# Performance work log

Measured on AMD Instinct MI355X. Metric: run time of the kernel, lower is better.

Reference implementation:

```python
import jax, jax.numpy as jnp
import numpy as np

D_MODEL = 1024
NUM_HEADS = 16
D_K = D_MODEL // NUM_HEADS


def setup_inputs() -> dict:
    key = jax.random.key(0)
    ks = jax.random.split(key, 9)
    s = 1.0 / np.sqrt(D_MODEL)
    x = jax.random.normal(ks[0], (2, 2048, D_MODEL), dtype=jnp.float32)
    Wq = jax.random.uniform(ks[1], (D_MODEL, D_MODEL), jnp.float32, -s, s)
    bq = jax.random.uniform(ks[2], (D_MODEL,), jnp.float32, -s, s)
    Wk = jax.random.uniform(ks[3], (D_MODEL, D_MODEL), jnp.float32, -s, s)
    bk = jax.random.uniform(ks[4], (D_MODEL,), jnp.float32, -s, s)
    Wv = jax.random.uniform(ks[5], (D_MODEL, D_MODEL), jnp.float32, -s, s)
    bv = jax.random.uniform(ks[6], (D_MODEL,), jnp.float32, -s, s)
    Wo = jax.random.uniform(ks[7], (D_MODEL, D_MODEL), jnp.float32, -s, s)
    bo = jax.random.uniform(ks[8], (D_MODEL,), jnp.float32, -s, s)
    return {"x": x, "Wq": Wq, "bq": bq, "Wk": Wk, "bk": bk,
            "Wv": Wv, "bv": bv, "Wo": Wo, "bo": bo}


def reference(x, Wq, bq, Wk, bk, Wv, bv, Wo, bo):
    B, S, _ = x.shape
    # projections (torch Linear: x @ W.T + b; here W stored as [in, out])
    q = (x @ Wq + bq).reshape(B, S, NUM_HEADS, D_K).transpose(0, 2, 1, 3)
    k = (x @ Wk + bk).reshape(B, S, NUM_HEADS, D_K).transpose(0, 2, 1, 3)
    v = (x @ Wv + bv).reshape(B, S, NUM_HEADS, D_K).transpose(0, 2, 1, 3)
    scores = jnp.einsum('bhqd,bhkd->bhqk', q, k) / jnp.sqrt(jnp.float32(D_K))
    attn = jax.nn.softmax(scores, axis=-1)
    out = jnp.einsum('bhqk,bhkd->bhqd', attn, v)  # [B,H,S,Dk]
    out = out.transpose(0, 2, 1, 3).reshape(B, S, D_MODEL)
    return out @ Wo + bo
```

## Files before the change

kernel.cpp:

```cpp
#include <hip/hip_runtime.h>
#include <hip/hip_bf16.h>

#define SEQ   2048
#define DM    1024
#define NH    16
#define DK    64
#define BATCH 2
#define M_TOT 4096
#define C1 0.18033688011112042f

typedef __attribute__((ext_vector_type(8))) short bf16x8;
typedef __attribute__((ext_vector_type(4))) float f32x4;
typedef unsigned short u16;

__device__ inline u16 f2b(float f) {
    union { float f; unsigned u; } x; x.f = f;
    return (u16)((x.u + 0x7FFFu + ((x.u >> 16) & 1u)) >> 16);
}

__device__ inline unsigned pk2(float a, float b) {
    __hip_bfloat162 h = __float22bfloat162_rn(make_float2(a, b));
    return *reinterpret_cast<unsigned*>(&h);
}

__device__ inline void async_cp16(const u16* g, u16* l) {
    __builtin_amdgcn_global_load_lds(
        (const __attribute__((address_space(1))) unsigned int*)g,
        (__attribute__((address_space(3))) unsigned int*)l, 16, 0, 0);
}

__global__ __launch_bounds__(256) void cast_x(
    const float4* __restrict__ x, uint2* __restrict__ xb)
{
    int gid = blockIdx.x * 256 + threadIdx.x;
    float4 v = x[gid];
    uint2 o;
    o.x = pk2(v.x, v.y); o.y = pk2(v.z, v.w);
    xb[gid] = o;
}

__global__ __launch_bounds__(256) void transpose_cast4(
    const float* __restrict__ W0, const float* __restrict__ W1,
    const float* __restrict__ W2, const float* __restrict__ W3,
    u16* __restrict__ WtBase)
{
    __shared__ float tile[32][33];
    const int t = threadIdx.x;
    const int n0 = blockIdx.x << 5, k0 = blockIdx.y << 5, z = blockIdx.z;
    const float* W = (z == 0) ? W0 : (z == 1) ? W1 : (z == 2) ? W2 : W3;
    u16* Wt = WtBase + (size_t)z * DM * DM;
    #pragma unroll
    for (int i = 0; i < 4; ++i) {
        int idx = t + (i << 8); int r = idx >> 5, c = idx & 31;
        tile[r][c] = W[(size_t)(k0 + r) * DM + n0 + c];
    }
    __syncthreads();
    #pragma unroll
    for (int i = 0; i < 4; ++i) {
        int idx = t + (i << 8); int r = idx >> 5, c = idx & 31;
        Wt[(size_t)(n0 + r) * DM + k0 + c] = f2b(tile[c][r]);
    }
}

__global__ __launch_bounds__(256) void gemm_bt(
    const u16* __restrict__ A, const u16* __restrict__ Bt, int mode,
    const float* __restrict__ bias0, const float* __restrict__ bias1,
    const float* __restrict__ bias2,
    void* __restrict__ out0, void* __restrict__ out1, void* __restrict__ out2)
{
    __shared__ u16 sh[9216];
    u16* As = sh;
    u16* Bs = sh + 4096;
    const int t = threadIdx.x, wid = t >> 6, lane = t & 63;
    const int lr = lane & 15, quad = lane >> 4;
    const int m0 = blockIdx.y << 7, n0 = blockIdx.x << 7;
    const int wm = (wid & 1) << 6, wn = (wid >> 1) << 6;
    const int rowA = lane >> 2;
    const int colA = (((lane & 3) - ((lane >> 3) & 3)) & 3) << 3;
    const int sA = (((lr >> 1) + quad) & 3) << 3;

    f32x4 acc[4][4];
    #pragma unroll
    for (int i = 0; i < 4; ++i)
        #pragma unroll
        for (int j = 0; j < 4; ++j) acc[i][j] = (f32x4){0.f, 0.f, 0.f, 0.f};

    for (int k0 = 0; k0 < DM; k0 += 32) {
        #pragma unroll
        for (int i = 0; i < 2; ++i) {
            int ch = wid * 2 + i;
            async_cp16(A  + (size_t)(m0 + ch * 16 + rowA) * DM + k0 + colA,
                       As + ch * 16 * 32);
            async_cp16(Bt + (size_t)(n0 + ch * 16 + rowA) * DM + k0 + colA,
                       Bs + ch * 16 * 32);
        }
        __syncthreads();
        bf16x8 af[4], bfr[4];
        #pragma unroll
        for (int mt = 0; mt < 4; ++mt)
            af[mt] = *(const bf16x8*)(As + (wm + 16 * mt + lr) * 32 + sA);
        #pragma unroll
        for (int nt = 0; nt < 4; ++nt)
            bfr[nt] = *(const bf16x8*)(Bs + (wn + 16 * nt + lr) * 32 + sA);
        #pragma unroll
        for (int mt = 0; mt < 4; ++mt)
            #pragma unroll
            for (int nt = 0; nt < 4; ++nt)
                acc[mt][nt] = __builtin_amdgcn_mfma_f32_16x16x32_bf16(
                    af[mt], bfr[nt], acc[mt][nt], 0, 0, 0);
        __syncthreads();
    }

    if (mode == 1) {
        u16* wstrip = sh + wid * 1152;
        const int ngb = n0 + wn;
        const int which = ngb >> 10, nnb = ngb & 1023;
        const int h = nnb >> 6;
        const float* bp = (which == 0) ? bias0 : (which == 1) ? bias1 : bias2;
        const float sc = (which == 0) ? C1 : 1.0f;
        float bias_v[4];
        #pragma unroll
        for (int nt = 0; nt < 4; ++nt) bias_v[nt] = bp[nnb + 16 * nt + lr];

        if (which != 1) {
            u16* dst = (which == 0) ? (u16*)out0 : (u16*)out2;
            #pragma unroll
            for (int mt = 0; mt < 4; ++mt) {
                #pragma unroll
                for (int nt = 0; nt < 4; ++nt) {
                    uint2 w;
                    w.x = pk2((acc[mt][nt][0] + bias_v[nt]) * sc,
                              (acc[mt][nt][1] + bias_v[nt]) * sc);
                    w.y = pk2((acc[mt][nt][2] + bias_v[nt]) * sc,
                              (acc[mt][nt][3] + bias_v[nt]) * sc);
                    *(uint2*)(wstrip + (16 * nt + lr) * 16 + quad * 4) = w;
                }
                asm volatile("s_waitcnt lgkmcnt(0)" ::: "memory");
                #pragma unroll
                for (int half = 0; half < 2; ++half) {
                    int id = lane + 64 * half;
                    int d = id >> 1, cho = (id & 1) << 3;
                    int m = m0 + wm + 16 * mt + cho;
                    int b = m >> 11, s = m & (SEQ - 1);
                    *(uint4*)(dst + ((size_t)(b * NH + h) * DK + d) * SEQ + s) =
                        *(const uint4*)(wstrip + d * 16 + cho);
                }
                asm volatile("s_waitcnt lgkmcnt(0)" ::: "memory");
            }
        } else {
            u16* dst = (u16*)out1;
            #pragma unroll
            for (int mt = 0; mt < 4; ++mt) {
                #pragma unroll
                for (int nt = 0; nt < 4; ++nt)
                    #pragma unroll
                    for (int r = 0; r < 4; ++r)
                        wstrip[(quad * 4 + r) * 72 + 16 * nt + lr] =
                            f2b(acc[mt][nt][r] + bias_v[nt]);
                asm volatile("s_waitcnt lgkmcnt(0)" ::: "memory");
                #pragma unroll
                for (int half = 0; half < 2; ++half) {
                    int id = lane + 64 * half;
                    int mloc = id >> 3, dl = (id & 7) << 3;
                    int m = m0 + wm + 16 * mt + mloc;
                    int b = m >> 11, s = m & (SEQ - 1);
                    *(uint4*)(dst + ((size_t)(b * NH + h) * SEQ + s) * DK + dl) =
                        *(const uint4*)(wstrip + mloc * 72 + dl);
                }
                asm volatile("s_waitcnt lgkmcnt(0)" ::: "memory");
            }
        }
    } else {
        float* O = (float*)out0;
        float* strip = (float*)sh + wid * 1088;
        float bias_v[4];
        #pragma unroll
        for (int nt = 0; nt < 4; ++nt) bias_v[nt] = bias0[n0 + wn + 16 * nt + lr];
        #pragma unroll
        for (int mt = 0; mt < 4; ++mt) {
            #pragma unroll
            for (int nt = 0; nt < 4; ++nt)
                #pragma unroll
                for (int r = 0; r < 4; ++r)
                    strip[(quad * 4 + r) * 68 + 16 * nt + lr] =
                        acc[mt][nt][r] + bias_v[nt];
            asm volatile("s_waitcnt lgkmcnt(0)" ::: "memory");
            #pragma unroll
            for (int rr = 0; rr < 4; ++rr) {
                int row = lane >> 2, chunk = (lane & 3) + 4 * rr;
                float4 v = *(const float4*)(strip + row * 68 + chunk * 4);
                *(float4*)(O + (size_t)(m0 + wm + 16 * mt + row) * DM
                             + n0 + wn + chunk * 4) = v;
            }
            asm volatile("s_waitcnt lgkmcnt(0)" ::: "memory");
        }
    }
}

__global__ __launch_bounds__(256) void attn_mfma(
    const u16* __restrict__ Qt, const u16* __restrict__ K,
    const u16* __restrict__ Vt, u16* __restrict__ A)
{
    __shared__ u16 sh[24576];

    const int t = threadIdx.x, wid = t >> 6, lane = t & 63;
    const int lr = lane & 15, quad = lane >> 4;
    const int bx = blockIdx.x;
    const int xcd = bx & 7, within = bx >> 3;
    const int bh  = xcd * 4 + (within >> 4);
    const int q0  = (within & 15) << 7;

    const u16* Kb = K  + (size_t)bh * SEQ * DK;
    const u16* Vb = Vt + (size_t)bh * DK * SEQ;

    const int qbase = q0 + 32 * wid + lr;
    const u16* Qb = Qt + (size_t)bh * DK * SEQ;
    bf16x8 bQ[2][2];
    #pragma unroll
    for (int g = 0; g < 2; ++g) {
        const u16* Qp = Qb + qbase + 16 * g;
        #pragma unroll
        for (int j = 0; j < 8; ++j) {
            bQ[g][0][j] = (short)Qp[(size_t)(quad * 8 + j) * SEQ];
            bQ[g][1][j] = (short)Qp[(size_t)(32 + quad * 8 + j) * SEQ];
        }
    }

    f32x4 O[2][4];
    #pragma unroll
    for (int g = 0; g < 2; ++g)
        #pragma unroll
        for (int mt = 0; mt < 4; ++mt) O[g][mt] = (f32x4){0.f, 0.f, 0.f, 0.f};
    float l_r[2] = {0.f, 0.f};

    const int srow = t >> 3;
    const int scol = (((t & 7) ^ (srow & 7)) << 3);

    const int c0 = ((quad ^ (lr & 7)) << 3);
    const int c1 = (((quad + 4) ^ (lr & 7)) << 3);
    const int prow = 16384 + wid * 2048 + lr * 64;

    auto stage = [&](int kt, int buf) {
        u16* kd = sh + (buf << 12);
        u16* vd = sh + 8192 + (buf << 12);
        async_cp16(Kb + (size_t)(kt + srow) * DK + scol,       kd + wid * 512);
        async_cp16(Kb + (size_t)(kt + srow + 32) * DK + scol,  kd + 2048 + wid * 512);
        async_cp16(Vb + (size_t)srow * SEQ + kt + scol,        vd + wid * 512);
        async_cp16(Vb + (size_t)(srow + 32) * SEQ + kt + scol, vd + 2048 + wid * 512);
    };

    stage(0, 0);
    __syncthreads();

    for (int it = 0; it < SEQ / 64; ++it) {
        const int kbase = (it & 1) << 12;
        const int vbase = 8192 + ((it & 1) << 12);
        if (it + 1 < SEQ / 64) stage((it + 1) << 6, (it + 1) & 1);

        #pragma unroll
        for (int mt = 0; mt < 4; ++mt) {
            bf16x8 a0 = *(const bf16x8*)(sh + kbase + (16 * mt + lr) * 64 + c0);
            bf16x8 a1 = *(const bf16x8*)(sh + kbase + (16 * mt + lr) * 64 + c1);
            #pragma unroll
            for (int g = 0; g < 2; ++g) {
                f32x4 s = (f32x4){0.f, 0.f, 0.f, 0.f};
                s = __builtin_amdgcn_mfma_f32_16x16x32_bf16(a0, bQ[g][0], s, 0, 0, 0);
                s = __builtin_amdgcn_mfma_f32_16x16x32_bf16(a1, bQ[g][1], s, 0, 0, 0);
                float e0 = __builtin_amdgcn_exp2f(s[0]);
                float e1 = __builtin_amdgcn_exp2f(s[1]);
                float e2 = __builtin_amdgcn_exp2f(s[2]);
                float e3 = __builtin_amdgcn_exp2f(s[3]);
                l_r[g] += (e0 + e1) + (e2 + e3);
                uint2 pk;
                pk.x = pk2(e0, e1); pk.y = pk2(e2, e3);
                int chunk = 2 * mt + (quad >> 1);
                *(uint2*)(sh + prow + (g << 10) + ((chunk ^ (lr & 7)) << 3)
                             + ((quad & 1) << 2)) = pk;
            }
        }
        asm volatile("s_waitcnt lgkmcnt(0)" ::: "memory");

        bf16x8 p00 = *(const bf16x8*)(sh + prow + c0);
        bf16x8 p01 = *(const bf16x8*)(sh + prow + c1);
        bf16x8 p10 = *(const bf16x8*)(sh + prow + 1024 + c0);
        bf16x8 p11 = *(const bf16x8*)(sh + prow + 1024 + c1);
        #pragma unroll
        for (int mt = 0; mt < 4; ++mt) {
            bf16x8 v0 = *(const bf16x8*)(sh + vbase + (16 * mt + lr) * 64 + c0);
            bf16x8 v1 = *(const bf16x8*)(sh + vbase + (16 * mt + lr) * 64 + c1);
            O[0][mt] = __builtin_amdgcn_mfma_f32_16x16x32_bf16(v0, p00, O[0][mt], 0, 0, 0);
            O[0][mt] = __builtin_amdgcn_mfma_f32_16x16x32_bf16(v1, p01, O[0][mt], 0, 0, 0);
            O[1][mt] = __builtin_amdgcn_mfma_f32_16x16x32_bf16(v0, p10, O[1][mt], 0, 0, 0);
            O[1][mt] = __builtin_amdgcn_mfma_f32_16x16x32_bf16(v1, p11, O[1][mt], 0, 0, 0);
        }
        if (it + 1 < SEQ / 64) __syncthreads();
    }

    #pragma unroll
    for (int g = 0; g < 2; ++g) {
        l_r[g] += __shfl_xor(l_r[g], 16);
        l_r[g] += __shfl_xor(l_r[g], 32);
    }

    const int b = bh >> 4, h = bh & 15;
    #pragma unroll
    for (int g = 0; g < 2; ++g) {
        float inv = 1.f / l_r[g];
        const int q = qbase + 16 * g;
        #pragma unroll
        for (int mt = 0; mt < 4; ++mt) {
            uint2 pk;
            pk.x = pk2(O[g][mt][0] * inv, O[g][mt][1] * inv);
            pk.y = pk2(O[g][mt][2] * inv, O[g][mt][3] * inv);
            *(uint2*)(A + (size_t)(b * SEQ + q) * DM + h * DK + 16 * mt + 4 * quad) = pk;
        }
    }
}

extern "C" void kernel_launch(void* const* d_in, const int* in_sizes, int n_in,
                              void* d_out, int out_size, void* d_ws, size_t ws_size,
                              hipStream_t stream)
{
    const float* x  = (const float*)d_in[0];
    const float* Wq = (const float*)d_in[1];
    const float* bq = (const float*)d_in[2];
    const float* Wk = (const float*)d_in[3];
    const float* bk = (const float*)d_in[4];
    const float* Wv = (const float*)d_in[5];
    const float* bv = (const float*)d_in[6];
    const float* Wo = (const float*)d_in[7];
    const float* bo = (const float*)d_in[8];

    const size_t NE = (size_t)M_TOT * DM;
    u16* xb     = (u16*)d_ws;
    u16* wt_qkv = xb + NE;
    u16* wt_o   = wt_qkv + 3 * (size_t)DM * DM;
    u16* qt_ws  = wt_o + (size_t)DM * DM;
    u16* k_ws   = qt_ws + NE;
    u16* vt_ws  = k_ws + NE;
    u16* a_ws   = vt_ws + NE;

    cast_x<<<M_TOT * DM / 4 / 256, 256, 0, stream>>>((const float4*)x, (uint2*)xb);
    transpose_cast4<<<dim3(32, 32, 4), 256, 0, stream>>>(Wq, Wk, Wv, Wo, wt_qkv);

    gemm_bt<<<dim3(24, 32), 256, 0, stream>>>(
        xb, wt_qkv, 1, bq, bk, bv, qt_ws, k_ws, vt_ws);

    attn_mfma<<<dim3(512), 256, 0, stream>>>(qt_ws, k_ws, vt_ws, a_ws);

    gemm_bt<<<dim3(8, 32), 256, 0, stream>>>(
        a_ws, wt_o, 0, bo, nullptr, nullptr, d_out, nullptr, nullptr);
}
```

Baseline: 217.3 us.

## Software-pipeline attention loop: overlap previous tile's PV MFMA with current QK

Restructures the attention main loop so each iteration first runs the P·V MFMAs for the previous tile, then the Q·K MFMAs for the current tile, with exp and the P write deferred until afterwards. The P buffer is double-buffered and V is triple-buffered to hold the extra tile in flight, with a final epilogue for the last PV step. s_setprio is raised around the MFMA block. The aim is to hide the exp/LDS-write latency behind matrix work and drop the mid-iteration lgkmcnt wait. In exchange it uses more LDS (72KB) and more registers, which may reduce occupancy.

Result: no change. 213.3 us (-1.8%).

```diff
diff --git a/kernel.cpp b/kernel.cpp
--- a/kernel.cpp
+++ b/kernel.cpp
@@ -201,7 +201,7 @@
     const u16* __restrict__ Qt, const u16* __restrict__ K,
     const u16* __restrict__ Vt, u16* __restrict__ A)
 {
-    __shared__ u16 sh[24576];
+    __shared__ u16 sh[36864];
 
     const int t = threadIdx.x, wid = t >> 6, lane = t & 63;
     const int lr = lane & 15, quad = lane >> 4;
@@ -238,62 +238,110 @@
 
     const int c0 = ((quad ^ (lr & 7)) << 3);
     const int c1 = (((quad + 4) ^ (lr & 7)) << 3);
-    const int prow = 16384 + wid * 2048 + lr * 64;
-
-    auto stage = [&](int kt, int buf) {
-        u16* kd = sh + (buf << 12);
-        u16* vd = sh + 8192 + (buf << 12);
+    const int pwave = 20480 + wid * 4096 + lr * 64;
+
+    auto stage = [&](int kt, int kbuf, int vbuf) {
+        u16* kd = sh + (kbuf << 12);
+        u16* vd = sh + 8192 + (vbuf << 12);
         async_cp16(Kb + (size_t)(kt + srow) * DK + scol,       kd + wid * 512);
         async_cp16(Kb + (size_t)(kt + srow + 32) * DK + scol,  kd + 2048 + wid * 512);
         async_cp16(Vb + (size_t)srow * SEQ + kt + scol,        vd + wid * 512);
         async_cp16(Vb + (size_t)(srow + 32) * SEQ + kt + scol, vd + 2048 + wid * 512);
     };
 
-    stage(0, 0);
+    stage(0, 0, 0);
     __syncthreads();
 
+    int vst = 1, vpv = 2;
     for (int it = 0; it < SEQ / 64; ++it) {
-        const int kbase = (it & 1) << 12;
-        const int vbase = 8192 + ((it & 1) << 12);
-        if (it + 1 < SEQ / 64) stage((it + 1) << 6, (it + 1) & 1);
-
-        #pragma unroll
-        for (int mt = 0; mt < 4; ++mt) {
-            bf16x8 a0 = *(const bf16x8*)(sh + kbase + (16 * mt + lr) * 64 + c0);
-            bf16x8 a1 = *(const bf16x8*)(sh + kbase + (16 * mt + lr) * 64 + c1);
+        if (it + 1 < SEQ / 64) stage((it + 1) << 6, (~it) & 1, vst);
+
+        bf16x8 p00, p01, p10, p11;
+        bf16x8 vf0[4], vf1[4];
+        if (it > 0) {
+            const int pr = pwave + (((~it) & 1) << 11);
+            p00 = *(const bf16x8*)(sh + pr + c0);
+            p01 = *(const bf16x8*)(sh + pr + c1);
+            p10 = *(const bf16x8*)(sh + pr + 1024 + c0);
+            p11 = *(const bf16x8*)(sh + pr + 1024 + c1);
+            const u16* vbp = sh + 8192 + (vpv << 12);
+            #pragma unroll
+            for (int mt = 0; mt < 4; ++mt) {
+                vf0[mt] = *(const bf16x8*)(vbp + (16 * mt + lr) * 64 + c0);
+                vf1[mt] = *(const bf16x8*)(vbp + (16 * mt + lr) * 64 + c1);
+            }
+        }
+
+        const u16* kbp = sh + ((it & 1) << 12);
+        bf16x8 a0[4], a1[4];
+        #pragma unroll
+        for (int mt = 0; mt < 4; ++mt) {
+            a0[mt] = *(const bf16x8*)(kbp + (16 * mt + lr) * 64 + c0);
+            a1[mt] = *(const bf16x8*)(kbp + (16 * mt + lr) * 64 + c1);
+        }
+
+        __builtin_amdgcn_s_setprio(1);
+        if (it > 0) {
+            #pragma unroll
+            for (int mt = 0; mt < 4; ++mt) {
+                O[0][mt] = __builtin_amdgcn_mfma_f32_16x16x32_bf16(vf0[mt], p00, O[0][mt], 0, 0, 0);
+                O[0][mt] = __builtin_amdgcn_mfma_f32_16x16x32_bf16(vf1[mt], p01, O[0][mt], 0, 0, 0);
+                O[1][mt] = __builtin_amdgcn_mfma_f32_16x16x32_bf16(vf0[mt], p10, O[1][mt], 0, 0, 0);
+                O[1][mt] = __builtin_amdgcn_mfma_f32_16x16x32_bf16(vf1[mt], p11, O[1][mt], 0, 0, 0);
+            }
+        }
+        f32x4 S[2][4];
+        #pragma unroll
+        for (int mt = 0; mt < 4; ++mt) {
             #pragma unroll
             for (int g = 0; g < 2; ++g) {
                 f32x4 s = (f32x4){0.f, 0.f, 0.f, 0.f};
-                s = __builtin_amdgcn_mfma_f32_16x16x32_bf16(a0, bQ[g][0], s, 0, 0, 0);
-                s = __builtin_amdgcn_mfma_f32_16x16x32_bf16(a1, bQ[g][1], s, 0, 0, 0);
-                float e0 = __builtin_amdgcn_exp2f(s[0]);
-                float e1 = __builtin_amdgcn_exp2f(s[1]);
-                float e2 = __builtin_amdgcn_exp2f(s[2]);
-                float e3 = __builtin_amdgcn_exp2f(s[3]);
+                s = __builtin_amdgcn_mfma_f32_16x16x32_bf16(a0[mt], bQ[g][0], s, 0, 0, 0);
+                s = __builtin_amdgcn_mfma_f32_16x16x32_bf16(a1[mt], bQ[g][1], s, 0, 0, 0);
+                S[g][mt] = s;
+            }
+        }
+        __builtin_amdgcn_s_setprio(0);
+
+        const int pw = pwave + ((it & 1) << 11);
+        #pragma unroll
+        for (int mt = 0; mt < 4; ++mt) {
+            #pragma unroll
+            for (int g = 0; g < 2; ++g) {
+                float e0 = __builtin_amdgcn_exp2f(S[g][mt][0]);
+                float e1 = __builtin_amdgcn_exp2f(S[g][mt][1]);
+                float e2 = __builtin_amdgcn_exp2f(S[g][mt][2]);
+                float e3 = __builtin_amdgcn_exp2f(S[g][mt][3]);
                 l_r[g] += (e0 + e1) + (e2 + e3);
                 uint2 pk;
                 pk.x = pk2(e0, e1); pk.y = pk2(e2, e3);
                 int chunk = 2 * mt + (quad >> 1);
-                *(uint2*)(sh + prow + (g << 10) + ((chunk ^ (lr & 7)) << 3)
+                *(uint2*)(sh + pw + (g << 10) + ((chunk ^ (lr & 7)) << 3)
                              + ((quad & 1) << 2)) = pk;
             }
         }
-        asm volatile("s_waitcnt lgkmcnt(0)" ::: "memory");
-
-        bf16x8 p00 = *(const bf16x8*)(sh + prow + c0);
-        bf16x8 p01 = *(const bf16x8*)(sh + prow + c1);
-        bf16x8 p10 = *(const bf16x8*)(sh + prow + 1024 + c0);
-        bf16x8 p11 = *(const bf16x8*)(sh + prow + 1024 + c1);
-        #pragma unroll
-        for (int mt = 0; mt < 4; ++mt) {
-            bf16x8 v0 = *(const bf16x8*)(sh + vbase + (16 * mt + lr) * 64 + c0);
-            bf16x8 v1 = *(const bf16x8*)(sh + vbase + (16 * mt + lr) * 64 + c1);
+
+        __syncthreads();
+        if (++vst == 3) vst = 0;
+        if (++vpv == 3) vpv = 0;
+    }
+
+    {
+        const int pr = pwave + (((SEQ / 64 - 1) & 1) << 11);
+        bf16x8 p00 = *(const bf16x8*)(sh + pr + c0);
+        bf16x8 p01 = *(const bf16x8*)(sh + pr + c1);
+        bf16x8 p10 = *(const bf16x8*)(sh + pr + 1024 + c0);
+        bf16x8 p11 = *(const bf16x8*)(sh + pr + 1024 + c1);
+        const u16* vbp = sh + 8192 + (((SEQ / 64 - 1) % 3) << 12);
+        #pragma unroll
+        for (int mt = 0; mt < 4; ++mt) {
+            bf16x8 v0 = *(const bf16x8*)(vbp + (16 * mt + lr) * 64 + c0);
+            bf16x8 v1 = *(const bf16x8*)(vbp + (16 * mt + lr) * 64 + c1);
             O[0][mt] = __builtin_amdgcn_mfma_f32_16x16x32_bf16(v0, p00, O[0][mt], 0, 0, 0);
             O[0][mt] = __builtin_amdgcn_mfma_f32_16x16x32_bf16(v1, p01, O[0][mt], 0, 0, 0);
             O[1][mt] = __builtin_amdgcn_mfma_f32_16x16x32_bf16(v0, p10, O[1][mt], 0, 0, 0);
             O[1][mt] = __builtin_amdgcn_mfma_f32_16x16x32_bf16(v1, p11, O[1][mt], 0, 0, 0);
         }
-        if (it + 1 < SEQ / 64) __syncthreads();
     }
 
     #pragma unroll
```

## Switch attention to 32x32x16 MFMA with register-resident P via permlane32 swap

Applied to the files above, without the earlier changes.

Rewrites the attention inner loop to use 32x32x16 bf16 MFMA tiles instead of 16x16x32. The softmax probabilities now stay in registers and are rearranged with permlane32_swap, so the P round-trip through LDS and its wait are gone and the LDS footprint shrinks. It also adds s_setprio around the MFMA phases. In exchange, each lane now holds larger accumulators, so register pressure rises, and the epilogue writes scalar 16-bit values through an LDS-staged row-sum table instead of packed stores.

After: 211.0 us. -2.9%, faster.

```diff
diff --git a/kernel.cpp b/kernel.cpp
--- a/kernel.cpp
+++ b/kernel.cpp
@@ -11,6 +11,8 @@
 
 typedef __attribute__((ext_vector_type(8))) short bf16x8;
 typedef __attribute__((ext_vector_type(4))) float f32x4;
+typedef __attribute__((ext_vector_type(16))) float f32x16;
+typedef __attribute__((ext_vector_type(2))) int i32x2;
 typedef unsigned short u16;
 
 __device__ inline u16 f2b(float f) {
@@ -28,6 +30,21 @@
         (const __attribute__((address_space(1))) unsigned int*)g,
         (__attribute__((address_space(3))) unsigned int*)l, 16, 0, 0);
 }
+
+__device__ inline f32x16 zero16() {
+    f32x16 z;
+    #pragma unroll
+    for (int i = 0; i < 16; ++i) z[i] = 0.f;
+    return z;
+}
+
+__device__ inline bf16x8 mk8(unsigned a, unsigned b, unsigned c, unsigned d) {
+    union { unsigned u[4]; bf16x8 v; } x;
+    x.u[0] = a; x.u[1] = b; x.u[2] = c; x.u[3] = d;
+    return x.v;
+}
+
+#define MFMA32(a, b, c) __builtin_amdgcn_mfma_f32_32x32x16_bf16(a, b, c, 0, 0, 0)
 
 __global__ __launch_bounds__(256) void cast_x(
     const float4* __restrict__ x, uint2* __restrict__ xb)
@@ -201,10 +218,10 @@
     const u16* __restrict__ Qt, const u16* __restrict__ K,
     const u16* __restrict__ Vt, u16* __restrict__ A)
 {
-    __shared__ u16 sh[24576];
+    __shared__ u16 sh[16640];
 
     const int t = threadIdx.x, wid = t >> 6, lane = t & 63;
-    const int lr = lane & 15, quad = lane >> 4;
+    const int l31 = lane & 31, hi = lane >> 5, l7 = lane & 7;
     const int bx = blockIdx.x;
     const int xcd = bx & 7, within = bx >> 3;
     const int bh  = xcd * 4 + (within >> 4);
@@ -213,32 +230,25 @@
     const u16* Kb = K  + (size_t)bh * SEQ * DK;
     const u16* Vb = Vt + (size_t)bh * DK * SEQ;
 
-    const int qbase = q0 + 32 * wid + lr;
-    const u16* Qb = Qt + (size_t)bh * DK * SEQ;
-    bf16x8 bQ[2][2];
-    #pragma unroll
-    for (int g = 0; g < 2; ++g) {
-        const u16* Qp = Qb + qbase + 16 * g;
-        #pragma unroll
-        for (int j = 0; j < 8; ++j) {
-            bQ[g][0][j] = (short)Qp[(size_t)(quad * 8 + j) * SEQ];
-            bQ[g][1][j] = (short)Qp[(size_t)(32 + quad * 8 + j) * SEQ];
-        }
-    }
-
-    f32x4 O[2][4];
-    #pragma unroll
-    for (int g = 0; g < 2; ++g)
-        #pragma unroll
-        for (int mt = 0; mt < 4; ++mt) O[g][mt] = (f32x4){0.f, 0.f, 0.f, 0.f};
-    float l_r[2] = {0.f, 0.f};
+    const int qw = q0 + 32 * wid + l31;
+    const u16* Qb = Qt + (size_t)bh * DK * SEQ + qw;
+    bf16x8 bQ[4];
+    #pragma unroll
+    for (int s = 0; s < 4; ++s)
+        #pragma unroll
+        for (int j = 0; j < 8; ++j)
+            bQ[s][j] = (short)Qb[(size_t)(16 * s + 8 * hi + j) * SEQ];
+
+    f32x16 O0 = zero16(), O1 = zero16();
+    float lr = 0.f;
 
     const int srow = t >> 3;
     const int scol = (((t & 7) ^ (srow & 7)) << 3);
 
-    const int c0 = ((quad ^ (lr & 7)) << 3);
-    const int c1 = (((quad + 4) ^ (lr & 7)) << 3);
-    const int prow = 16384 + wid * 2048 + lr * 64;
+    const int rA = l31 * 64;
+    int cks[4];
+    #pragma unroll
+    for (int s = 0; s < 4; ++s) cks[s] = ((2 * s + hi) ^ l7) << 3;
 
     auto stage = [&](int kt, int buf) {
         u16* kd = sh + (buf << 12);
@@ -253,67 +263,83 @@
     __syncthreads();
 
     for (int it = 0; it < SEQ / 64; ++it) {
-        const int kbase = (it & 1) << 12;
-        const int vbase = 8192 + ((it & 1) << 12);
+        const u16* kbp = sh + ((it & 1) << 12) + rA;
+        const u16* vbp = sh + 8192 + ((it & 1) << 12) + rA;
         if (it + 1 < SEQ / 64) stage((it + 1) << 6, (it + 1) & 1);
 
-        #pragma unroll
-        for (int mt = 0; mt < 4; ++mt) {
-            bf16x8 a0 = *(const bf16x8*)(sh + kbase + (16 * mt + lr) * 64 + c0);
-            bf16x8 a1 = *(const bf16x8*)(sh + kbase + (16 * mt + lr) * 64 + c1);
-            #pragma unroll
-            for (int g = 0; g < 2; ++g) {
-                f32x4 s = (f32x4){0.f, 0.f, 0.f, 0.f};
-                s = __builtin_amdgcn_mfma_f32_16x16x32_bf16(a0, bQ[g][0], s, 0, 0, 0);
-                s = __builtin_amdgcn_mfma_f32_16x16x32_bf16(a1, bQ[g][1], s, 0, 0, 0);
-                float e0 = __builtin_amdgcn_exp2f(s[0]);
-                float e1 = __builtin_amdgcn_exp2f(s[1]);
-                float e2 = __builtin_amdgcn_exp2f(s[2]);
-                float e3 = __builtin_amdgcn_exp2f(s[3]);
-                l_r[g] += (e0 + e1) + (e2 + e3);
-                uint2 pk;
-                pk.x = pk2(e0, e1); pk.y = pk2(e2, e3);
-                int chunk = 2 * mt + (quad >> 1);
-                *(uint2*)(sh + prow + (g << 10) + ((chunk ^ (lr & 7)) << 3)
-                             + ((quad & 1) << 2)) = pk;
+        f32x16 Sv[2];
+        __builtin_amdgcn_s_setprio(1);
+        {
+            bf16x8 a;
+            f32x16 s0 = zero16();
+            a = *(const bf16x8*)(kbp + cks[0]); s0 = MFMA32(a, bQ[0], s0);
+            a = *(const bf16x8*)(kbp + cks[1]); s0 = MFMA32(a, bQ[1], s0);
+            a = *(const bf16x8*)(kbp + cks[2]); s0 = MFMA32(a, bQ[2], s0);
+            a = *(const bf16x8*)(kbp + cks[3]); s0 = MFMA32(a, bQ[3], s0);
+            Sv[0] = s0;
+            f32x16 s1 = zero16();
+            a = *(const bf16x8*)(kbp + 2048 + cks[0]); s1 = MFMA32(a, bQ[0], s1);
+            a = *(const bf16x8*)(kbp + 2048 + cks[1]); s1 = MFMA32(a, bQ[1], s1);
+            a = *(const bf16x8*)(kbp + 2048 + cks[2]); s1 = MFMA32(a, bQ[2], s1);
+            a = *(const bf16x8*)(kbp + 2048 + cks[3]); s1 = MFMA32(a, bQ[3], s1);
+            Sv[1] = s1;
+        }
+        __builtin_amdgcn_s_setprio(0);
+
+        unsigned pa[4][4];
+        #pragma unroll
+        for (int kvt = 0; kvt < 2; ++kvt) {
+            float e[16];
+            #pragma unroll
+            for (int r = 0; r < 16; ++r)
+                e[r] = __builtin_amdgcn_exp2f(Sv[kvt][r]);
+            lr += (((e[0] + e[1]) + (e[2] + e[3])) +
+                   ((e[4] + e[5]) + (e[6] + e[7]))) +
+                  (((e[8] + e[9]) + (e[10] + e[11])) +
+                   ((e[12] + e[13]) + (e[14] + e[15])));
+            unsigned pk8[8];
+            #pragma unroll
+            for (int i = 0; i < 8; ++i) pk8[i] = pk2(e[2 * i], e[2 * i + 1]);
+            #pragma unroll
+            for (int ww = 0; ww < 2; ++ww) {
+                i32x2 r0 = __builtin_amdgcn_permlane32_swap(
+                    (int)pk8[4 * ww + 0], (int)pk8[4 * ww + 2], false, false);
+                i32x2 r1 = __builtin_amdgcn_permlane32_swap(
+                    (int)pk8[4 * ww + 1], (int)pk8[4 * ww + 3], false, false);
+                const int w = 2 * kvt + ww;
+                pa[w][0] = (unsigned)r0[0]; pa[w][1] = (unsigned)r1[0];
+                pa[w][2] = (unsigned)r0[1]; pa[w][3] = (unsigned)r1[1];
             }
         }
-        asm volatile("s_waitcnt lgkmcnt(0)" ::: "memory");
-
-        bf16x8 p00 = *(const bf16x8*)(sh + prow + c0);
-        bf16x8 p01 = *(const bf16x8*)(sh + prow + c1);
-        bf16x8 p10 = *(const bf16x8*)(sh + prow + 1024 + c0);
-        bf16x8 p11 = *(const bf16x8*)(sh + prow + 1024 + c1);
-        #pragma unroll
-        for (int mt = 0; mt < 4; ++mt) {
-            bf16x8 v0 = *(const bf16x8*)(sh + vbase + (16 * mt + lr) * 64 + c0);
-            bf16x8 v1 = *(const bf16x8*)(sh + vbase + (16 * mt + lr) * 64 + c1);
-            O[0][mt] = __builtin_amdgcn_mfma_f32_16x16x32_bf16(v0, p00, O[0][mt], 0, 0, 0);
-            O[0][mt] = __builtin_amdgcn_mfma_f32_16x16x32_bf16(v1, p01, O[0][mt], 0, 0, 0);
-            O[1][mt] = __builtin_amdgcn_mfma_f32_16x16x32_bf16(v0, p10, O[1][mt], 0, 0, 0);
-            O[1][mt] = __builtin_amdgcn_mfma_f32_16x16x32_bf16(v1, p11, O[1][mt], 0, 0, 0);
-        }
-        if (it + 1 < SEQ / 64) __syncthreads();
-    }
-
-    #pragma unroll
-    for (int g = 0; g < 2; ++g) {
-        l_r[g] += __shfl_xor(l_r[g], 16);
-        l_r[g] += __shfl_xor(l_r[g], 32);
-    }
+
+        __builtin_amdgcn_s_setprio(1);
+        #pragma unroll
+        for (int w = 0; w < 4; ++w) {
+            bf16x8 pw = mk8(pa[w][0], pa[w][1], pa[w][2], pa[w][3]);
+            bf16x8 v0 = *(const bf16x8*)(vbp + cks[w]);
+            bf16x8 v1 = *(const bf16x8*)(vbp + 2048 + cks[w]);
+            O0 = MFMA32(pw, v0, O0);
+            O1 = MFMA32(pw, v1, O1);
+        }
+        __builtin_amdgcn_s_setprio(0);
+
+        __syncthreads();
+    }
+
+    lr += __shfl_xor(lr, 32);
+    float* lt = (float*)(sh + 16384) + wid * 32;
+    lt[l31] = lr;
+    asm volatile("s_waitcnt lgkmcnt(0)" ::: "memory");
 
     const int b = bh >> 4, h = bh & 15;
-    #pragma unroll
-    for (int g = 0; g < 2; ++g) {
-        float inv = 1.f / l_r[g];
-        const int q = qbase + 16 * g;
-        #pragma unroll
-        for (int mt = 0; mt < 4; ++mt) {
-            uint2 pk;
-            pk.x = pk2(O[g][mt][0] * inv, O[g][mt][1] * inv);
-            pk.y = pk2(O[g][mt][2] * inv, O[g][mt][3] * inv);
-            *(uint2*)(A + (size_t)(b * SEQ + q) * DM + h * DK + 16 * mt + 4 * quad) = pk;
-        }
+    u16* Ab = A + (size_t)b * SEQ * DM + h * DK + l31;
+    #pragma unroll
+    for (int r = 0; r < 16; ++r) {
+        const int qr = (r & 3) + 8 * (r >> 2) + 4 * hi;
+        const float inv = 1.f / lt[qr];
+        u16* dst = Ab + (size_t)(q0 + 32 * wid + qr) * DM;
+        dst[0]  = f2b(O0[r] * inv);
+        dst[32] = f2b(O1[r] * inv);
     }
 }
 
```
